# Kernel optimization log

Measured on AMD Instinct MI355X. Metric: run time of the kernel, lower is better.

Reference implementation:

```python
import jax, jax.numpy as jnp
import numpy as np

N_NODES = 50000
N_EDGES = 800000
D = 128          # embedding_dim
G = 3            # group_size
K = 4            # window_size
ALPHA = -0.5
WEIGHTS = (1.0, 1.0, 7.81, 45.28)
EPS = 1e-12      # torch F.normalize clamp_min


def _striped_projection(key):
    """Striped sparse random projection, densified (matches torch coalesce+to_dense)."""
    num_groups = D // G  # 42; columns 126..127 remain zero, as in the original
    k_off, k_sign = jax.random.split(key)
    row_idx = jnp.repeat(jnp.arange(N_NODES), num_groups)
    base = jnp.tile(jnp.arange(0, num_groups * G, G), N_NODES)
    off = jax.random.randint(k_off, (N_NODES * num_groups,), 0, G)
    col_idx = base + off
    scale = float(np.sqrt(G))  # 1/sqrt(density), density = 1/g
    vals = (jax.random.randint(k_sign, (N_NODES * num_groups,), 0, 2).astype(jnp.float32) * 2.0 - 1.0) * scale
    return jnp.zeros((N_NODES, D), jnp.float32).at[row_idx, col_idx].add(vals)


def setup_inputs() -> dict:
    key = jax.random.key(0)
    k1, k2, k3 = jax.random.split(key, 3)
    edge_row = jax.random.randint(k1, (N_EDGES,), 0, N_NODES)
    edge_col = jax.random.randint(k2, (N_EDGES,), 0, N_NODES)
    edge_val = jnp.ones((N_EDGES,), jnp.float32)
    R = _striped_projection(k3)
    return {"edge_row": edge_row, "edge_col": edge_col, "edge_val": edge_val, "R": R}


def reference(edge_row, edge_col, edge_val, R):
    N = R.shape[0]
    # degrees = row sums of sparse adjacency; zeros -> 1
    deg = jax.ops.segment_sum(edge_val, edge_row, num_segments=N)
    deg = jnp.where(deg == 0, 1.0, deg)
    # initial degree scaling: N_curr = R * deg**alpha
    x = R * (deg ** ALPHA)[:, None]
    inv_deg = (1.0 / deg)[:, None]
    acc = jnp.zeros_like(R)
    for i in range(K):
        # SpMM: out[r] = sum_{e: row[e]==r} val[e] * x[col[e]]
        x = jax.ops.segment_sum(edge_val[:, None] * x[edge_col], edge_row, num_segments=N)
        x = x * inv_deg  # transition-matrix ('trans') scaling
        nrm = jnp.maximum(jnp.sqrt(jnp.sum(x * x, axis=1, keepdims=True)), EPS)
        acc = acc + (x / nrm) * WEIGHTS[i]
    mean = acc.mean(axis=0)
    std = jnp.std(acc, axis=0, ddof=1)  # torch .std() is unbiased
    std = jnp.where(std == 0, 1.0, std)
    return (acc - mean) / std
```

## Files before the change

### kernel.cpp

```cpp
#include <hip/hip_runtime.h>
#include <math.h>

#define NN 50000
#define NE 800000
#define DD 128
#define NBKT 196
#define BCAP 5120
#define CHUNK 2048
#define NCHUNK ((NE + CHUNK - 1) / CHUNK)
#define CS1_NBLK 1024
#define CS_ROWS 49

static __device__ __forceinline__ float blo(unsigned int p) { return __uint_as_float(p << 16); }
static __device__ __forceinline__ float bhi(unsigned int p) { return __uint_as_float(p & 0xffff0000u); }
static __device__ __forceinline__ unsigned int pack2bf(float a, float b) {
    unsigned int ua = __float_as_uint(a);
    unsigned int ub = __float_as_uint(b);
    ua = ua + 0x7FFFu + ((ua >> 16) & 1u);
    ub = ub + 0x7FFFu + ((ub >> 16) & 1u);
    return (ua >> 16) | (ub & 0xffff0000u);
}

static __global__ __launch_bounds__(256) void bin_kernel(
    const int* __restrict__ erow, const int* __restrict__ ecol, const float* __restrict__ eval_,
    int* __restrict__ bucket_cursor, uint2* __restrict__ binned) {
    __shared__ uint2 sorted[CHUNK];
    __shared__ unsigned short sbin[CHUNK];
    __shared__ int hist[NBKT];
    __shared__ int bstart[NBKT];
    __shared__ int bcur[NBKT];
    __shared__ int gbase[NBKT];
    __shared__ int tmp[256];

    int t = threadIdx.x;
    int cbase = blockIdx.x * CHUNK;
    int cn = NE - cbase; if (cn > CHUNK) cn = CHUNK;

    for (int i = t; i < NBKT; i += 256) hist[i] = 0;
    __syncthreads();

    unsigned int rc[8]; unsigned int vv[8]; int bb[8];
    int nloc = 0;
    for (int i = t; i < cn; i += 256) {
        int g = cbase + i;
        int r = erow[g];
        int c = ecol[g];
        float v = eval_[g];
        rc[nloc] = (unsigned)r | ((unsigned)c << 16);
        vv[nloc] = __float_as_uint(v);
        int b = r >> 8;
        bb[nloc] = b;
        atomicAdd(&hist[b], 1);
        ++nloc;
    }
    __syncthreads();

    int hv = (t < NBKT) ? hist[t] : 0;
    tmp[t] = hv;
    __syncthreads();
    for (int off = 1; off < 256; off <<= 1) {
        int u = (t >= off) ? tmp[t - off] : 0;
        __syncthreads();
        tmp[t] += u;
        __syncthreads();
    }
    if (t < NBKT) {
        int ex = tmp[t] - hv;
        bstart[t] = ex;
        bcur[t] = ex;
        gbase[t] = atomicAdd(&bucket_cursor[t], hv);
    }
    __syncthreads();

    for (int k = 0; k < nloc; ++k) {
        int pos = atomicAdd(&bcur[bb[k]], 1);
        sorted[pos] = make_uint2(rc[k], vv[k]);
        sbin[pos] = (unsigned short)bb[k];
    }
    __syncthreads();

    for (int i = t; i < cn; i += 256) {
        int b = sbin[i];
        binned[(size_t)b * BCAP + gbase[b] + (i - bstart[b])] = sorted[i];
    }
}

static __global__ void bucket_scan_kernel(const int* __restrict__ bucket_cursor,
                                          int* __restrict__ bucket_base) {
    __shared__ int tmp[256];
    int t = threadIdx.x;
    int v = (t < NBKT) ? bucket_cursor[t] : 0;
    tmp[t] = v;
    __syncthreads();
    for (int off = 1; off < 256; off <<= 1) {
        int u = (t >= off) ? tmp[t - off] : 0;
        __syncthreads();
        tmp[t] += u;
        __syncthreads();
    }
    if (t < NBKT) bucket_base[t] = tmp[t] - v;
}

static __global__ __launch_bounds__(256) void sort_kernel(
    const uint2* __restrict__ binned, const int* __restrict__ bucket_cursor,
    const int* __restrict__ bucket_base, uint2* __restrict__ csr, int* __restrict__ row_start,
    float* __restrict__ deg) {
    __shared__ uint2 buf[BCAP];
    __shared__ int hist[256];
    __shared__ int rcur[256];
    __shared__ float fdeg[256];
    int b = blockIdx.x;
    int t = threadIdx.x;
    int cnt = bucket_cursor[b];
    int gb = bucket_base[b];
    int lo = b << 8;

    hist[t] = 0;
    fdeg[t] = 0.0f;
    __syncthreads();
    for (int i = t; i < cnt; i += 256) {
        uint2 e = binned[(size_t)b * BCAP + i];
        buf[i] = e;
        int rr = (int)(e.x & 0xFFFFu) - lo;
        atomicAdd(&hist[rr], 1);
        atomicAdd(&fdeg[rr], __uint_as_float(e.y));
    }
    __syncthreads();
    int hv = hist[t];
    rcur[t] = hv;
    __syncthreads();
    for (int off = 1; off < 256; off <<= 1) {
        int u = (t >= off) ? rcur[t - off] : 0;
        __syncthreads();
        rcur[t] += u;
        __syncthreads();
    }
    int excl = rcur[t] - hv;
    int r = lo + t;
    if (r < NN) {
        row_start[r] = gb + excl;
        float d = fdeg[t];
        deg[r] = (d == 0.0f) ? 1.0f : d;
    }
    if (b == NBKT - 1 && t == 255) row_start[NN] = gb + cnt;
    rcur[t] = excl;
    __syncthreads();
    for (int i = t; i < cnt; i += 256) {
        uint2 e = buf[i];
        int rr = (int)(e.x & 0xFFFFu) - lo;
        int pos = atomicAdd(&rcur[rr], 1);
        csr[(size_t)gb + pos] = make_uint2(e.x >> 16, e.y);
    }
}

static __global__ void init_x_kernel(const float* __restrict__ R, const float* __restrict__ deg,
                                     uint4* __restrict__ xq, int nquads) {
    int i = blockIdx.x * blockDim.x + threadIdx.x;
    if (i < nquads) {
        float d = deg[i >> 4];
        float sc = rsqrtf(d);
        const float4* R4 = (const float4*)R;
        float4 f0 = R4[i * 2];
        float4 f1 = R4[i * 2 + 1];
        xq[i] = make_uint4(pack2bf(f0.x * sc, f0.y * sc), pack2bf(f0.z * sc, f0.w * sc),
                           pack2bf(f1.x * sc, f1.y * sc), pack2bf(f1.z * sc, f1.w * sc));
    }
}

static __global__ __launch_bounds__(256) void spmm_fused_kernel(
    const int* __restrict__ row_start, const uint2* __restrict__ csr,
    const uint4* __restrict__ x4, const float* __restrict__ deg,
    uint4* __restrict__ x_next4, float* __restrict__ s_out, float weight) {
    int wave = threadIdx.x >> 6;
    int lane = threadIdx.x & 63;
    int quarter = lane >> 4;
    int sub = lane & 15;
    int row = blockIdx.x * 16 + wave * 4 + quarter;
    int s = row_start[row];
    int e = row_start[row + 1];

    float a0 = 0.f, a1 = 0.f, a2 = 0.f, a3 = 0.f, a4 = 0.f, a5 = 0.f, a6 = 0.f, a7 = 0.f;
    for (int base = s; base < e; base += 16) {
        int j = base + sub;
        int cl = 0;
        float vl = 0.0f;
        if (j < e) { uint2 t2 = csr[j]; cl = (int)t2.x; vl = __uint_as_float(t2.y); }
        int cnt = e - base; if (cnt > 16) cnt = 16;
        for (int k = 0; k < cnt; k += 4) {
            int l0 = quarter * 16 + k;
            int c0 = __shfl(cl, l0);
            int c1 = __shfl(cl, l0 + 1);
            int c2 = __shfl(cl, l0 + 2);
            int c3 = __shfl(cl, l0 + 3);
            float v0 = __shfl(vl, l0);
            float v1 = __shfl(vl, l0 + 1);
            float v2 = __shfl(vl, l0 + 2);
            float v3 = __shfl(vl, l0 + 3);
            uint4 p0 = x4[(size_t)c0 * 16 + sub];
            uint4 p1 = x4[(size_t)c1 * 16 + sub];
            uint4 p2 = x4[(size_t)c2 * 16 + sub];
            uint4 p3 = x4[(size_t)c3 * 16 + sub];
            a0 += v0 * blo(p0.x); a1 += v0 * bhi(p0.x); a2 += v0 * blo(p0.y); a3 += v0 * bhi(p0.y);
            a4 += v0 * blo(p0.z); a5 += v0 * bhi(p0.z); a6 += v0 * blo(p0.w); a7 += v0 * bhi(p0.w);
            a0 += v1 * blo(p1.x); a1 += v1 * bhi(p1.x); a2 += v1 * blo(p1.y); a3 += v1 * bhi(p1.y);
            a4 += v1 * blo(p1.z); a5 += v1 * bhi(p1.z); a6 += v1 * blo(p1.w); a7 += v1 * bhi(p1.w);
            a0 += v2 * blo(p2.x); a1 += v2 * bhi(p2.x); a2 += v2 * blo(p2.y); a3 += v2 * bhi(p2.y);
            a4 += v2 * blo(p2.z); a5 += v2 * bhi(p2.z); a6 += v2 * blo(p2.w); a7 += v2 * bhi(p2.w);
            a0 += v3 * blo(p3.x); a1 += v3 * bhi(p3.x); a2 += v3 * blo(p3.y); a3 += v3 * bhi(p3.y);
            a4 += v3 * blo(p3.z); a5 += v3 * bhi(p3.z); a6 += v3 * blo(p3.w); a7 += v3 * bhi(p3.w);
        }
    }

    float id = 1.0f / deg[row];
    a0 *= id; a1 *= id; a2 *= id; a3 *= id; a4 *= id; a5 *= id; a6 *= id; a7 *= id;

    float ss = a0 * a0 + a1 * a1 + a2 * a2 + a3 * a3 + a4 * a4 + a5 * a5 + a6 * a6 + a7 * a7;
#pragma unroll
    for (int m = 1; m <= 8; m <<= 1) ss += __shfl_xor(ss, m);
    float nrm = fmaxf(sqrtf(ss), 1e-12f);

    x_next4[(size_t)row * 16 + sub] = make_uint4(pack2bf(a0, a1), pack2bf(a2, a3),
                                                 pack2bf(a4, a5), pack2bf(a6, a7));
    if (sub == 0) s_out[row] = weight / nrm;
}

static __global__ __launch_bounds__(256) void stats_kernel(
    const uint4* __restrict__ x1, const uint4* __restrict__ x2,
    const uint4* __restrict__ x3, const uint4* __restrict__ x4,
    const float* __restrict__ s1, const float* __restrict__ s2,
    const float* __restrict__ s3, const float* __restrict__ s4,
    double* __restrict__ psum, double* __restrict__ psumsq) {
    __shared__ double shs[256 * 8];
    __shared__ double shq[256 * 8];
    int t = threadIdx.x;
    int sub = t & 15;
    int ro = t >> 4;
    int rbeg = blockIdx.x * CS_ROWS;
    int rend = rbeg + CS_ROWS; if (rend > NN) rend = NN;

    double ls[8], lq[8];
#pragma unroll
    for (int j = 0; j < 8; ++j) { ls[j] = 0.0; lq[j] = 0.0; }

    for (int r = rbeg + ro; r < rend; r += 16) {
        float w1 = s1[r], w2 = s2[r], w3 = s3[r], w4 = s4[r];
        size_t xi = (size_t)r * 16 + sub;
        uint4 q1 = x1[xi], q2 = x2[xi], q3 = x3[xi], q4 = x4[xi];
        float v[8];
        v[0] = w1 * blo(q1.x) + w2 * blo(q2.x) + w3 * blo(q3.x) + w4 * blo(q4.x);
        v[1] = w1 * bhi(q1.x) + w2 * bhi(q2.x) + w3 * bhi(q3.x) + w4 * bhi(q4.x);
        v[2] = w1 * blo(q1.y) + w2 * blo(q2.y) + w3 * blo(q3.y) + w4 * blo(q4.y);
        v[3] = w1 * bhi(q1.y) + w2 * bhi(q2.y) + w3 * bhi(q3.y) + w4 * bhi(q4.y);
        v[4] = w1 * blo(q1.z) + w2 * blo(q2.z) + w3 * blo(q3.z) + w4 * blo(q4.z);
        v[5] = w1 * bhi(q1.z) + w2 * bhi(q2.z) + w3 * bhi(q3.z) + w4 * bhi(q4.z);
        v[6] = w1 * blo(q1.w) + w2 * blo(q2.w) + w3 * blo(q3.w) + w4 * blo(q4.w);
        v[7] = w1 * bhi(q1.w) + w2 * bhi(q2.w) + w3 * bhi(q3.w) + w4 * bhi(q4.w);
#pragma unroll
        for (int j = 0; j < 8; ++j) { ls[j] += (double)v[j]; lq[j] += (double)v[j] * (double)v[j]; }
    }
#pragma unroll
    for (int j = 0; j < 8; ++j) { shs[t * 8 + j] = ls[j]; shq[t * 8 + j] = lq[j]; }
    __syncthreads();
    if (t < DD) {
        int cs = t >> 3, cj = t & 7;
        double s = 0.0, q = 0.0;
        for (int g = 0; g < 16; ++g) {
            int src = (g * 16 + cs) * 8 + cj;
            s += shs[src];
            q += shq[src];
        }
        psum[(size_t)blockIdx.x * DD + t] = s;
        psumsq[(size_t)blockIdx.x * DD + t] = q;
    }
}

static __global__ __launch_bounds__(256) void colstats_fold_kernel(
    const double* __restrict__ psum, const double* __restrict__ psumsq,
    float* __restrict__ mean, float* __restrict__ invstd) {
    __shared__ double ss[256], qq[256];
    int c = blockIdx.x;
    int t = threadIdx.x;
    double s = 0.0, q = 0.0;
    for (int b = t; b < CS1_NBLK; b += 256) {
        s += psum[(size_t)b * DD + c];
        q += psumsq[(size_t)b * DD + c];
    }
    ss[t] = s; qq[t] = q;
    __syncthreads();
    for (int off = 128; off > 0; off >>= 1) {
        if (t < off) { ss[t] += ss[t + off]; qq[t] += qq[t + off]; }
        __syncthreads();
    }
    if (t == 0) {
        double m = ss[0] / (double)NN;
        double var = (qq[0] - (double)NN * m * m) / (double)(NN - 1);
        if (var < 0.0) var = 0.0;
        double sd = sqrt(var);
        if (sd == 0.0) sd = 1.0;
        mean[c] = (float)m;
        invstd[c] = (float)(1.0 / sd);
    }
}

static __global__ __launch_bounds__(256) void final_kernel(
    const uint4* __restrict__ x1, const uint4* __restrict__ x2,
    const uint4* __restrict__ x3, const uint4* __restrict__ x4,
    const float* __restrict__ s1, const float* __restrict__ s2,
    const float* __restrict__ s3, const float* __restrict__ s4,
    const float* __restrict__ mean, const float* __restrict__ invstd,
    float* __restrict__ out) {
    int i = blockIdx.x * blockDim.x + threadIdx.x;
    int r = i >> 4;
    int sub = i & 15;
    float w1 = s1[r], w2 = s2[r], w3 = s3[r], w4 = s4[r];
    uint4 q1 = x1[i], q2 = x2[i], q3 = x3[i], q4 = x4[i];
    float v[8];
    v[0] = w1 * blo(q1.x) + w2 * blo(q2.x) + w3 * blo(q3.x) + w4 * blo(q4.x);
    v[1] = w1 * bhi(q1.x) + w2 * bhi(q2.x) + w3 * bhi(q3.x) + w4 * bhi(q4.x);
    v[2] = w1 * blo(q1.y) + w2 * blo(q2.y) + w3 * blo(q3.y) + w4 * blo(q4.y);
    v[3] = w1 * bhi(q1.y) + w2 * bhi(q2.y) + w3 * bhi(q3.y) + w4 * bhi(q4.y);
    v[4] = w1 * blo(q1.z) + w2 * blo(q2.z) + w3 * blo(q3.z) + w4 * blo(q4.z);
    v[5] = w1 * bhi(q1.z) + w2 * bhi(q2.z) + w3 * bhi(q3.z) + w4 * bhi(q4.z);
    v[6] = w1 * blo(q1.w) + w2 * blo(q2.w) + w3 * blo(q3.w) + w4 * blo(q4.w);
    v[7] = w1 * bhi(q1.w) + w2 * bhi(q2.w) + w3 * bhi(q3.w) + w4 * bhi(q4.w);
    const float4* m4 = (const float4*)mean;
    const float4* is4 = (const float4*)invstd;
    float4 m0 = m4[sub * 2], m1 = m4[sub * 2 + 1];
    float4 i0 = is4[sub * 2], i1 = is4[sub * 2 + 1];
    float4* out4 = (float4*)out;
    out4[(size_t)i * 2]     = make_float4((v[0] - m0.x) * i0.x, (v[1] - m0.y) * i0.y,
                                          (v[2] - m0.z) * i0.z, (v[3] - m0.w) * i0.w);
    out4[(size_t)i * 2 + 1] = make_float4((v[4] - m1.x) * i1.x, (v[5] - m1.y) * i1.y,
                                          (v[6] - m1.z) * i1.z, (v[7] - m1.w) * i1.w);
}

extern "C" void kernel_launch(void* const* d_in, const int* in_sizes, int n_in,
                              void* d_out, int out_size, void* d_ws, size_t ws_size,
                              hipStream_t stream) {
    const int* erow = (const int*)d_in[0];
    const int* ecol = (const int*)d_in[1];
    const float* eval_ = (const float*)d_in[2];
    const float* R = (const float*)d_in[3];
    float* out = (float*)d_out;

    char* ws = (char*)d_ws;
    size_t off = 0;
    auto alloc = [&](size_t bytes) -> char* {
        char* p = ws + off;
        off += (bytes + 255) & ~(size_t)255;
        return p;
    };
    float* deg          = (float*)alloc(NN * sizeof(float));
    int* bucket_cursor  = (int*)alloc(NBKT * sizeof(int));
    int* bucket_base    = (int*)alloc(NBKT * sizeof(int));
    int* row_start      = (int*)alloc((NN + 1) * sizeof(int));
    uint2* binned       = (uint2*)alloc((size_t)NBKT * BCAP * sizeof(uint2));
    uint2* csr          = (uint2*)alloc((size_t)NE * sizeof(uint2));
    uint4* x0           = (uint4*)alloc((size_t)NN * 16 * sizeof(uint4));
    uint4* x1           = (uint4*)alloc((size_t)NN * 16 * sizeof(uint4));
    uint4* x2           = (uint4*)alloc((size_t)NN * 16 * sizeof(uint4));
    uint4* x3           = (uint4*)alloc((size_t)NN * 16 * sizeof(uint4));
    uint4* x4           = (uint4*)alloc((size_t)NN * 16 * sizeof(uint4));
    float* s1           = (float*)alloc(NN * sizeof(float));
    float* s2           = (float*)alloc(NN * sizeof(float));
    float* s3           = (float*)alloc(NN * sizeof(float));
    float* s4           = (float*)alloc(NN * sizeof(float));
    double* psum        = (double*)alloc((size_t)CS1_NBLK * DD * sizeof(double));
    double* psumsq      = (double*)alloc((size_t)CS1_NBLK * DD * sizeof(double));
    float* meanbuf      = (float*)alloc(DD * sizeof(float));
    float* invstdb      = (float*)alloc(DD * sizeof(float));

    hipMemsetAsync(bucket_cursor, 0, NBKT * sizeof(int), stream);

    const int total = NN * DD;
    const int nquads = total / 8;

    bin_kernel<<<NCHUNK, 256, 0, stream>>>(erow, ecol, eval_, bucket_cursor, binned);
    bucket_scan_kernel<<<1, 256, 0, stream>>>(bucket_cursor, bucket_base);
    sort_kernel<<<NBKT, 256, 0, stream>>>(binned, bucket_cursor, bucket_base, csr, row_start, deg);

    init_x_kernel<<<(nquads + 255) / 256, 256, 0, stream>>>(R, deg, x0, nquads);

    spmm_fused_kernel<<<NN / 16, 256, 0, stream>>>(row_start, csr, x0, deg, x1, s1, 1.0f);
    spmm_fused_kernel<<<NN / 16, 256, 0, stream>>>(row_start, csr, x1, deg, x2, s2, 1.0f);
    spmm_fused_kernel<<<NN / 16, 256, 0, stream>>>(row_start, csr, x2, deg, x3, s3, 7.81f);
    spmm_fused_kernel<<<NN / 16, 256, 0, stream>>>(row_start, csr, x3, deg, x4, s4, 45.28f);

    stats_kernel<<<CS1_NBLK, 256, 0, stream>>>(x1, x2, x3, x4, s1, s2, s3, s4, psum, psumsq);
    colstats_fold_kernel<<<DD, 256, 0, stream>>>(psum, psumsq, meanbuf, invstdb);
    final_kernel<<<NN * 16 / 256, 256, 0, stream>>>(x1, x2, x3, x4, s1, s2, s3, s4,
                                                    meanbuf, invstdb, out);
}
```

Measured before the change: 253.4 us.

## Fuse bucket scan and x0 init into sort; fuse stats and accumulation into last SpMM

Each sort block now computes the bucket prefix scan itself and writes its own rows of the degree-scaled bf16 x0, so the separate scan and init kernels go away. The last SpMM iteration builds the weighted sum of all four hops in place of storing x4. It writes the unnormalized result to out and emits per-block float column partial sums. A light normalize pass then rescales out in place, removing the extra re-reads of x1..x4 by the separate stats and final kernels. The per-block partials are now float instead of double, which may cost a little accuracy in the variance.

```diff
diff --git a/kernel.cpp b/kernel.cpp
--- a/kernel.cpp
+++ b/kernel.cpp
@@ -8,8 +8,7 @@
 #define BCAP 5120
 #define CHUNK 2048
 #define NCHUNK ((NE + CHUNK - 1) / CHUNK)
-#define CS1_NBLK 1024
-#define CS_ROWS 49
+#define SPMM_NBLK (NN / 16)
 
 static __device__ __forceinline__ float blo(unsigned int p) { return __uint_as_float(p << 16); }
 static __device__ __forceinline__ float bhi(unsigned int p) { return __uint_as_float(p & 0xffff0000u); }
@@ -85,39 +84,33 @@
     }
 }
 
-static __global__ void bucket_scan_kernel(const int* __restrict__ bucket_cursor,
-                                          int* __restrict__ bucket_base) {
-    __shared__ int tmp[256];
-    int t = threadIdx.x;
-    int v = (t < NBKT) ? bucket_cursor[t] : 0;
-    tmp[t] = v;
-    __syncthreads();
-    for (int off = 1; off < 256; off <<= 1) {
-        int u = (t >= off) ? tmp[t - off] : 0;
-        __syncthreads();
-        tmp[t] += u;
-        __syncthreads();
-    }
-    if (t < NBKT) bucket_base[t] = tmp[t] - v;
-}
-
 static __global__ __launch_bounds__(256) void sort_kernel(
     const uint2* __restrict__ binned, const int* __restrict__ bucket_cursor,
-    const int* __restrict__ bucket_base, uint2* __restrict__ csr, int* __restrict__ row_start,
-    float* __restrict__ deg) {
+    uint2* __restrict__ csr, int* __restrict__ row_start, float* __restrict__ deg,
+    const float* __restrict__ R, uint4* __restrict__ x0) {
     __shared__ uint2 buf[BCAP];
     __shared__ int hist[256];
     __shared__ int rcur[256];
     __shared__ float fdeg[256];
+    __shared__ int pscan[256];
     int b = blockIdx.x;
     int t = threadIdx.x;
-    int cnt = bucket_cursor[b];
-    int gb = bucket_base[b];
     int lo = b << 8;
 
+    int pv = (t < NBKT) ? bucket_cursor[t] : 0;
+    pscan[t] = pv;
     hist[t] = 0;
     fdeg[t] = 0.0f;
     __syncthreads();
+    for (int off = 1; off < 256; off <<= 1) {
+        int u = (t >= off) ? pscan[t - off] : 0;
+        __syncthreads();
+        pscan[t] += u;
+        __syncthreads();
+    }
+    int gb = (b == 0) ? 0 : pscan[b - 1];
+    int cnt = pscan[b] - gb;
+
     for (int i = t; i < cnt; i += 256) {
         uint2 e = binned[(size_t)b * BCAP + i];
         buf[i] = e;
@@ -151,18 +144,19 @@
         int pos = atomicAdd(&rcur[rr], 1);
         csr[(size_t)gb + pos] = make_uint2(e.x >> 16, e.y);
     }
-}
-
-static __global__ void init_x_kernel(const float* __restrict__ R, const float* __restrict__ deg,
-                                     uint4* __restrict__ xq, int nquads) {
-    int i = blockIdx.x * blockDim.x + threadIdx.x;
-    if (i < nquads) {
-        float d = deg[i >> 4];
+
+    int nrows = NN - lo; if (nrows > 256) nrows = 256;
+    const float4* __restrict__ R4 = (const float4*)R;
+    for (int idx = t; idx < nrows * 16; idx += 256) {
+        int rr = idx >> 4;
+        int sub = idx & 15;
+        float d = fdeg[rr];
+        d = (d == 0.0f) ? 1.0f : d;
         float sc = rsqrtf(d);
-        const float4* R4 = (const float4*)R;
-        float4 f0 = R4[i * 2];
-        float4 f1 = R4[i * 2 + 1];
-        xq[i] = make_uint4(pack2bf(f0.x * sc, f0.y * sc), pack2bf(f0.z * sc, f0.w * sc),
+        size_t g = (size_t)(lo + rr) * 16 + sub;
+        float4 f0 = R4[g * 2];
+        float4 f1 = R4[g * 2 + 1];
+        x0[g] = make_uint4(pack2bf(f0.x * sc, f0.y * sc), pack2bf(f0.z * sc, f0.w * sc),
                            pack2bf(f1.x * sc, f1.y * sc), pack2bf(f1.z * sc, f1.w * sc));
     }
 }
@@ -224,66 +218,110 @@
     if (sub == 0) s_out[row] = weight / nrm;
 }
 
-static __global__ __launch_bounds__(256) void stats_kernel(
-    const uint4* __restrict__ x1, const uint4* __restrict__ x2,
-    const uint4* __restrict__ x3, const uint4* __restrict__ x4,
-    const float* __restrict__ s1, const float* __restrict__ s2,
-    const float* __restrict__ s3, const float* __restrict__ s4,
-    double* __restrict__ psum, double* __restrict__ psumsq) {
-    __shared__ double shs[256 * 8];
-    __shared__ double shq[256 * 8];
+static __global__ __launch_bounds__(256) void spmm_last_kernel(
+    const int* __restrict__ row_start, const uint2* __restrict__ csr,
+    const uint4* __restrict__ xin, const float* __restrict__ deg,
+    const uint4* __restrict__ x1, const uint4* __restrict__ x2, const uint4* __restrict__ x3,
+    const float* __restrict__ s1, const float* __restrict__ s2, const float* __restrict__ s3,
+    float* __restrict__ out, float* __restrict__ psum, float* __restrict__ psumsq, float weight) {
+    __shared__ float shs[256 * 8];
+    __shared__ float shq[256 * 8];
+    int wave = threadIdx.x >> 6;
+    int lane = threadIdx.x & 63;
+    int quarter = lane >> 4;
+    int sub = lane & 15;
+    int row = blockIdx.x * 16 + wave * 4 + quarter;
+    int s = row_start[row];
+    int e = row_start[row + 1];
+
+    float a0 = 0.f, a1 = 0.f, a2 = 0.f, a3 = 0.f, a4 = 0.f, a5 = 0.f, a6 = 0.f, a7 = 0.f;
+    for (int base = s; base < e; base += 16) {
+        int j = base + sub;
+        int cl = 0;
+        float vl = 0.0f;
+        if (j < e) { uint2 t2 = csr[j]; cl = (int)t2.x; vl = __uint_as_float(t2.y); }
+        int cnt = e - base; if (cnt > 16) cnt = 16;
+        for (int k = 0; k < cnt; k += 4) {
+            int l0 = quarter * 16 + k;
+            int c0 = __shfl(cl, l0);
+            int c1 = __shfl(cl, l0 + 1);
+            int c2 = __shfl(cl, l0 + 2);
+            int c3 = __shfl(cl, l0 + 3);
+            float v0 = __shfl(vl, l0);
+            float v1 = __shfl(vl, l0 + 1);
+            float v2 = __shfl(vl, l0 + 2);
+            float v3 = __shfl(vl, l0 + 3);
+            uint4 p0 = xin[(size_t)c0 * 16 + sub];
+            uint4 p1 = xin[(size_t)c1 * 16 + sub];
+            uint4 p2 = xin[(size_t)c2 * 16 + sub];
+            uint4 p3 = xin[(size_t)c3 * 16 + sub];
+            a0 += v0 * blo(p0.x); a1 += v0 * bhi(p0.x); a2 += v0 * blo(p0.y); a3 += v0 * bhi(p0.y);
+            a4 += v0 * blo(p0.z); a5 += v0 * bhi(p0.z); a6 += v0 * blo(p0.w); a7 += v0 * bhi(p0.w);
+            a0 += v1 * blo(p1.x); a1 += v1 * bhi(p1.x); a2 += v1 * blo(p1.y); a3 += v1 * bhi(p1.y);
+            a4 += v1 * blo(p1.z); a5 += v1 * bhi(p1.z); a6 += v1 * blo(p1.w); a7 += v1 * bhi(p1.w);
+            a0 += v2 * blo(p2.x); a1 += v2 * bhi(p2.x); a2 += v2 * blo(p2.y); a3 += v2 * bhi(p2.y);
+            a4 += v2 * blo(p2.z); a5 += v2 * bhi(p2.z); a6 += v2 * blo(p2.w); a7 += v2 * bhi(p2.w);
+            a0 += v3 * blo(p3.x); a1 += v3 * bhi(p3.x); a2 += v3 * blo(p3.y); a3 += v3 * bhi(p3.y);
+            a4 += v3 * blo(p3.z); a5 += v3 * bhi(p3.z); a6 += v3 * blo(p3.w); a7 += v3 * bhi(p3.w);
+        }
+    }
+
+    float id = 1.0f / deg[row];
+    a0 *= id; a1 *= id; a2 *= id; a3 *= id; a4 *= id; a5 *= id; a6 *= id; a7 *= id;
+
+    float ss = a0 * a0 + a1 * a1 + a2 * a2 + a3 * a3 + a4 * a4 + a5 * a5 + a6 * a6 + a7 * a7;
+#pragma unroll
+    for (int m = 1; m <= 8; m <<= 1) ss += __shfl_xor(ss, m);
+    float nrm = fmaxf(sqrtf(ss), 1e-12f);
+    float w4 = weight / nrm;
+
+    size_t xi = (size_t)row * 16 + sub;
+    float w1 = s1[row], w2 = s2[row], w3 = s3[row];
+    uint4 q1 = x1[xi], q2 = x2[xi], q3 = x3[xi];
+    float v[8];
+    v[0] = w1 * blo(q1.x) + w2 * blo(q2.x) + w3 * blo(q3.x) + w4 * a0;
+    v[1] = w1 * bhi(q1.x) + w2 * bhi(q2.x) + w3 * bhi(q3.x) + w4 * a1;
+    v[2] = w1 * blo(q1.y) + w2 * blo(q2.y) + w3 * blo(q3.y) + w4 * a2;
+    v[3] = w1 * bhi(q1.y) + w2 * bhi(q2.y) + w3 * bhi(q3.y) + w4 * a3;
+    v[4] = w1 * blo(q1.z) + w2 * blo(q2.z) + w3 * blo(q3.z) + w4 * a4;
+    v[5] = w1 * bhi(q1.z) + w2 * bhi(q2.z) + w3 * bhi(q3.z) + w4 * a5;
+    v[6] = w1 * blo(q1.w) + w2 * blo(q2.w) + w3 * blo(q3.w) + w4 * a6;
+    v[7] = w1 * bhi(q1.w) + w2 * bhi(q2.w) + w3 * bhi(q3.w) + w4 * a7;
+
+    float4* out4 = (float4*)out;
+    out4[(size_t)row * 32 + sub * 2]     = make_float4(v[0], v[1], v[2], v[3]);
+    out4[(size_t)row * 32 + sub * 2 + 1] = make_float4(v[4], v[5], v[6], v[7]);
+
     int t = threadIdx.x;
-    int sub = t & 15;
-    int ro = t >> 4;
-    int rbeg = blockIdx.x * CS_ROWS;
-    int rend = rbeg + CS_ROWS; if (rend > NN) rend = NN;
-
-    double ls[8], lq[8];
 #pragma unroll
-    for (int j = 0; j < 8; ++j) { ls[j] = 0.0; lq[j] = 0.0; }
-
-    for (int r = rbeg + ro; r < rend; r += 16) {
-        float w1 = s1[r], w2 = s2[r], w3 = s3[r], w4 = s4[r];
-        size_t xi = (size_t)r * 16 + sub;
-        uint4 q1 = x1[xi], q2 = x2[xi], q3 = x3[xi], q4 = x4[xi];
-        float v[8];
-        v[0] = w1 * blo(q1.x) + w2 * blo(q2.x) + w3 * blo(q3.x) + w4 * blo(q4.x);
-        v[1] = w1 * bhi(q1.x) + w2 * bhi(q2.x) + w3 * bhi(q3.x) + w4 * bhi(q4.x);
-        v[2] = w1 * blo(q1.y) + w2 * blo(q2.y) + w3 * blo(q3.y) + w4 * blo(q4.y);
-        v[3] = w1 * bhi(q1.y) + w2 * bhi(q2.y) + w3 * bhi(q3.y) + w4 * bhi(q4.y);
-        v[4] = w1 * blo(q1.z) + w2 * blo(q2.z) + w3 * blo(q3.z) + w4 * blo(q4.z);
-        v[5] = w1 * bhi(q1.z) + w2 * bhi(q2.z) + w3 * bhi(q3.z) + w4 * bhi(q4.z);
-        v[6] = w1 * blo(q1.w) + w2 * blo(q2.w) + w3 * blo(q3.w) + w4 * blo(q4.w);
-        v[7] = w1 * bhi(q1.w) + w2 * bhi(q2.w) + w3 * bhi(q3.w) + w4 * bhi(q4.w);
-#pragma unroll
-        for (int j = 0; j < 8; ++j) { ls[j] += (double)v[j]; lq[j] += (double)v[j] * (double)v[j]; }
-    }
-#pragma unroll
-    for (int j = 0; j < 8; ++j) { shs[t * 8 + j] = ls[j]; shq[t * 8 + j] = lq[j]; }
+    for (int j = 0; j < 8; ++j) {
+        shs[t * 8 + j] = v[j];
+        shq[t * 8 + j] = v[j] * v[j];
+    }
     __syncthreads();
     if (t < DD) {
         int cs = t >> 3, cj = t & 7;
-        double s = 0.0, q = 0.0;
+        float sacc = 0.0f, qacc = 0.0f;
         for (int g = 0; g < 16; ++g) {
             int src = (g * 16 + cs) * 8 + cj;
-            s += shs[src];
-            q += shq[src];
+            sacc += shs[src];
+            qacc += shq[src];
         }
-        psum[(size_t)blockIdx.x * DD + t] = s;
-        psumsq[(size_t)blockIdx.x * DD + t] = q;
-    }
-}
-
-static __global__ __launch_bounds__(256) void colstats_fold_kernel(
-    const double* __restrict__ psum, const double* __restrict__ psumsq,
+        psum[(size_t)blockIdx.x * DD + t] = sacc;
+        psumsq[(size_t)blockIdx.x * DD + t] = qacc;
+    }
+}
+
+static __global__ __launch_bounds__(256) void fold_kernel(
+    const float* __restrict__ psum, const float* __restrict__ psumsq,
     float* __restrict__ mean, float* __restrict__ invstd) {
     __shared__ double ss[256], qq[256];
     int c = blockIdx.x;
     int t = threadIdx.x;
     double s = 0.0, q = 0.0;
-    for (int b = t; b < CS1_NBLK; b += 256) {
-        s += psum[(size_t)b * DD + c];
-        q += psumsq[(size_t)b * DD + c];
+    for (int b = t; b < SPMM_NBLK; b += 256) {
+        s += (double)psum[(size_t)b * DD + c];
+        q += (double)psumsq[(size_t)b * DD + c];
     }
     ss[t] = s; qq[t] = q;
     __syncthreads();
@@ -302,36 +340,19 @@
     }
 }
 
-static __global__ __launch_bounds__(256) void final_kernel(
-    const uint4* __restrict__ x1, const uint4* __restrict__ x2,
-    const uint4* __restrict__ x3, const uint4* __restrict__ x4,
-    const float* __restrict__ s1, const float* __restrict__ s2,
-    const float* __restrict__ s3, const float* __restrict__ s4,
-    const float* __restrict__ mean, const float* __restrict__ invstd,
-    float* __restrict__ out) {
+static __global__ __launch_bounds__(256) void normalize_kernel(
+    float* __restrict__ out, const float* __restrict__ mean, const float* __restrict__ invstd) {
     int i = blockIdx.x * blockDim.x + threadIdx.x;
-    int r = i >> 4;
-    int sub = i & 15;
-    float w1 = s1[r], w2 = s2[r], w3 = s3[r], w4 = s4[r];
-    uint4 q1 = x1[i], q2 = x2[i], q3 = x3[i], q4 = x4[i];
-    float v[8];
-    v[0] = w1 * blo(q1.x) + w2 * blo(q2.x) + w3 * blo(q3.x) + w4 * blo(q4.x);
-    v[1] = w1 * bhi(q1.x) + w2 * bhi(q2.x) + w3 * bhi(q3.x) + w4 * bhi(q4.x);
-    v[2] = w1 * blo(q1.y) + w2 * blo(q2.y) + w3 * blo(q3.y) + w4 * blo(q4.y);
-    v[3] = w1 * bhi(q1.y) + w2 * bhi(q2.y) + w3 * bhi(q3.y) + w4 * bhi(q4.y);
-    v[4] = w1 * blo(q1.z) + w2 * blo(q2.z) + w3 * blo(q3.z) + w4 * blo(q4.z);
-    v[5] = w1 * bhi(q1.z) + w2 * bhi(q2.z) + w3 * bhi(q3.z) + w4 * bhi(q4.z);
-    v[6] = w1 * blo(q1.w) + w2 * blo(q2.w) + w3 * blo(q3.w) + w4 * blo(q4.w);
-    v[7] = w1 * bhi(q1.w) + w2 * bhi(q2.w) + w3 * bhi(q3.w) + w4 * bhi(q4.w);
-    const float4* m4 = (const float4*)mean;
-    const float4* is4 = (const float4*)invstd;
-    float4 m0 = m4[sub * 2], m1 = m4[sub * 2 + 1];
-    float4 i0 = is4[sub * 2], i1 = is4[sub * 2 + 1];
+    int c4 = i & 31;
+    float4 m = ((const float4*)mean)[c4];
+    float4 is = ((const float4*)invstd)[c4];
     float4* out4 = (float4*)out;
-    out4[(size_t)i * 2]     = make_float4((v[0] - m0.x) * i0.x, (v[1] - m0.y) * i0.y,
-                                          (v[2] - m0.z) * i0.z, (v[3] - m0.w) * i0.w);
-    out4[(size_t)i * 2 + 1] = make_float4((v[4] - m1.x) * i1.x, (v[5] - m1.y) * i1.y,
-                                          (v[6] - m1.z) * i1.z, (v[7] - m1.w) * i1.w);
+    float4 v = out4[i];
+    v.x = (v.x - m.x) * is.x;
+    v.y = (v.y - m.y) * is.y;
+    v.z = (v.z - m.z) * is.z;
+    v.w = (v.w - m.w) * is.w;
+    out4[i] = v;
 }
 
 extern "C" void kernel_launch(void* const* d_in, const int* in_sizes, int n_in,
@@ -352,7 +373,6 @@
     };
     float* deg          = (float*)alloc(NN * sizeof(float));
     int* bucket_cursor  = (int*)alloc(NBKT * sizeof(int));
-    int* bucket_base    = (int*)alloc(NBKT * sizeof(int));
     int* row_start      = (int*)alloc((NN + 1) * sizeof(int));
     uint2* binned       = (uint2*)alloc((size_t)NBKT * BCAP * sizeof(uint2));
     uint2* csr          = (uint2*)alloc((size_t)NE * sizeof(uint2));
@@ -360,34 +380,25 @@
     uint4* x1           = (uint4*)alloc((size_t)NN * 16 * sizeof(uint4));
     uint4* x2           = (uint4*)alloc((size_t)NN * 16 * sizeof(uint4));
     uint4* x3           = (uint4*)alloc((size_t)NN * 16 * sizeof(uint4));
-    uint4* x4           = (uint4*)alloc((size_t)NN * 16 * sizeof(uint4));
     float* s1           = (float*)alloc(NN * sizeof(float));
     float* s2           = (float*)alloc(NN * sizeof(float));
     float* s3           = (float*)alloc(NN * sizeof(float));
-    float* s4           = (float*)alloc(NN * sizeof(float));
-    double* psum        = (double*)alloc((size_t)CS1_NBLK * DD * sizeof(double));
-    double* psumsq      = (double*)alloc((size_t)CS1_NBLK * DD * sizeof(double));
+    float* psum         = (float*)alloc((size_t)SPMM_NBLK * DD * sizeof(float));
+    float* psumsq       = (float*)alloc((size_t)SPMM_NBLK * DD * sizeof(float));
     float* meanbuf      = (float*)alloc(DD * sizeof(float));
     float* invstdb      = (float*)alloc(DD * sizeof(float));
 
     hipMemsetAsync(bucket_cursor, 0, NBKT * sizeof(int), stream);
 
-    const int total = NN * DD;
-    const int nquads = total / 8;
-
     bin_kernel<<<NCHUNK, 256, 0, stream>>>(erow, ecol, eval_, bucket_cursor, binned);
-    bucket_scan_kernel<<<1, 256, 0, stream>>>(bucket_cursor, bucket_base);
-    sort_kernel<<<NBKT, 256, 0, stream>>>(binned, bucket_cursor, bucket_base, csr, row_start, deg);
-
-    init_x_kernel<<<(nquads + 255) / 256, 256, 0, stream>>>(R, deg, x0, nquads);
-
-    spmm_fused_kernel<<<NN / 16, 256, 0, stream>>>(row_start, csr, x0, deg, x1, s1, 1.0f);
-    spmm_fused_kernel<<<NN / 16, 256, 0, stream>>>(row_start, csr, x1, deg, x2, s2, 1.0f);
-    spmm_fused_kernel<<<NN / 16, 256, 0, stream>>>(row_start, csr, x2, deg, x3, s3, 7.81f);
-    spmm_fused_kernel<<<NN / 16, 256, 0, stream>>>(row_start, csr, x3, deg, x4, s4, 45.28f);
-
-    stats_kernel<<<CS1_NBLK, 256, 0, stream>>>(x1, x2, x3, x4, s1, s2, s3, s4, psum, psumsq);
-    colstats_fold_kernel<<<DD, 256, 0, stream>>>(psum, psumsq, meanbuf, invstdb);
-    final_kernel<<<NN * 16 / 256, 256, 0, stream>>>(x1, x2, x3, x4, s1, s2, s3, s4,
-                                                    meanbuf, invstdb, out);
-}
+    sort_kernel<<<NBKT, 256, 0, stream>>>(binned, bucket_cursor, csr, row_start, deg, R, x0);
+
+    spmm_fused_kernel<<<SPMM_NBLK, 256, 0, stream>>>(row_start, csr, x0, deg, x1, s1, 1.0f);
+    spmm_fused_kernel<<<SPMM_NBLK, 256, 0, stream>>>(row_start, csr, x1, deg, x2, s2, 1.0f);
+    spmm_fused_kernel<<<SPMM_NBLK, 256, 0, stream>>>(row_start, csr, x2, deg, x3, s3, 7.81f);
+    spmm_last_kernel<<<SPMM_NBLK, 256, 0, stream>>>(row_start, csr, x3, deg, x1, x2, x3,
+                                                    s1, s2, s3, out, psum, psumsq, 45.28f);
+
+    fold_kernel<<<DD, 256, 0, stream>>>(psum, psumsq, meanbuf, invstdb);
+    normalize_kernel<<<NN * 32 / 256, 256, 0, stream>>>(out, meanbuf, invstdb);
+}
```

After: 252.0 us. About the same (-0.6%).

## Split SpMM into column slices, fold bucket scan and init into sort kernel

Applied to the files above, without the earlier changes.

The SpMM is restructured so each row is handled by 4 lanes, and the grid is split into 4 column slices of 32 features each. Within a launch, each slice gathers only a quarter of every source row, which is meant to shrink the working set and improve L2 reuse. Per-slice partial squared norms are written out and combined by a new small kernel that computes the per-row scale factors. Separately, the bucket prefix scan and the x0 initialisation are folded into the sort kernel, and the output stores become nontemporal. The cost is that each slice re-reads the CSR indices, and the extra partial-norm buffer adds memory traffic.

```diff
diff --git a/kernel.cpp b/kernel.cpp
--- a/kernel.cpp
+++ b/kernel.cpp
@@ -8,8 +8,12 @@
 #define BCAP 5120
 #define CHUNK 2048
 #define NCHUNK ((NE + CHUNK - 1) / CHUNK)
+#define NSLICE 4
+#define RB ((NN + 63) / 64)
 #define CS1_NBLK 1024
 #define CS_ROWS 49
+
+typedef unsigned int uiv4 __attribute__((ext_vector_type(4)));
 
 static __device__ __forceinline__ float blo(unsigned int p) { return __uint_as_float(p << 16); }
 static __device__ __forceinline__ float bhi(unsigned int p) { return __uint_as_float(p & 0xffff0000u); }
@@ -85,39 +89,33 @@
     }
 }
 
-static __global__ void bucket_scan_kernel(const int* __restrict__ bucket_cursor,
-                                          int* __restrict__ bucket_base) {
-    __shared__ int tmp[256];
-    int t = threadIdx.x;
-    int v = (t < NBKT) ? bucket_cursor[t] : 0;
-    tmp[t] = v;
-    __syncthreads();
-    for (int off = 1; off < 256; off <<= 1) {
-        int u = (t >= off) ? tmp[t - off] : 0;
-        __syncthreads();
-        tmp[t] += u;
-        __syncthreads();
-    }
-    if (t < NBKT) bucket_base[t] = tmp[t] - v;
-}
-
 static __global__ __launch_bounds__(256) void sort_kernel(
     const uint2* __restrict__ binned, const int* __restrict__ bucket_cursor,
-    const int* __restrict__ bucket_base, uint2* __restrict__ csr, int* __restrict__ row_start,
-    float* __restrict__ deg) {
+    uint2* __restrict__ csr, int* __restrict__ row_start, float* __restrict__ deg,
+    const float* __restrict__ R, uint4* __restrict__ x0) {
     __shared__ uint2 buf[BCAP];
     __shared__ int hist[256];
     __shared__ int rcur[256];
     __shared__ float fdeg[256];
+    __shared__ int pscan[256];
     int b = blockIdx.x;
     int t = threadIdx.x;
-    int cnt = bucket_cursor[b];
-    int gb = bucket_base[b];
     int lo = b << 8;
 
+    int pv = (t < NBKT) ? bucket_cursor[t] : 0;
+    pscan[t] = pv;
     hist[t] = 0;
     fdeg[t] = 0.0f;
     __syncthreads();
+    for (int off = 1; off < 256; off <<= 1) {
+        int u = (t >= off) ? pscan[t - off] : 0;
+        __syncthreads();
+        pscan[t] += u;
+        __syncthreads();
+    }
+    int gb = (b == 0) ? 0 : pscan[b - 1];
+    int cnt = pscan[b] - gb;
+
     for (int i = t; i < cnt; i += 256) {
         uint2 e = binned[(size_t)b * BCAP + i];
         buf[i] = e;
@@ -151,63 +149,76 @@
         int pos = atomicAdd(&rcur[rr], 1);
         csr[(size_t)gb + pos] = make_uint2(e.x >> 16, e.y);
     }
-}
-
-static __global__ void init_x_kernel(const float* __restrict__ R, const float* __restrict__ deg,
-                                     uint4* __restrict__ xq, int nquads) {
-    int i = blockIdx.x * blockDim.x + threadIdx.x;
-    if (i < nquads) {
-        float d = deg[i >> 4];
+
+    int nrows = NN - lo; if (nrows > 256) nrows = 256;
+    const float4* __restrict__ R4 = (const float4*)R;
+    for (int idx = t; idx < nrows * 16; idx += 256) {
+        int rr = idx >> 4;
+        int sub = idx & 15;
+        float d = fdeg[rr];
+        d = (d == 0.0f) ? 1.0f : d;
         float sc = rsqrtf(d);
-        const float4* R4 = (const float4*)R;
-        float4 f0 = R4[i * 2];
-        float4 f1 = R4[i * 2 + 1];
-        xq[i] = make_uint4(pack2bf(f0.x * sc, f0.y * sc), pack2bf(f0.z * sc, f0.w * sc),
+        size_t g = (size_t)(lo + rr) * 16 + sub;
+        float4 f0 = R4[g * 2];
+        float4 f1 = R4[g * 2 + 1];
+        x0[g] = make_uint4(pack2bf(f0.x * sc, f0.y * sc), pack2bf(f0.z * sc, f0.w * sc),
                            pack2bf(f1.x * sc, f1.y * sc), pack2bf(f1.z * sc, f1.w * sc));
     }
 }
 
-static __global__ __launch_bounds__(256) void spmm_fused_kernel(
+static __global__ __launch_bounds__(256) void spmm_slice_kernel(
     const int* __restrict__ row_start, const uint2* __restrict__ csr,
-    const uint4* __restrict__ x4, const float* __restrict__ deg,
-    uint4* __restrict__ x_next4, float* __restrict__ s_out, float weight) {
-    int wave = threadIdx.x >> 6;
-    int lane = threadIdx.x & 63;
-    int quarter = lane >> 4;
-    int sub = lane & 15;
-    int row = blockIdx.x * 16 + wave * 4 + quarter;
+    const uint4* __restrict__ xin, const float* __restrict__ deg,
+    uint4* __restrict__ xout, float* __restrict__ ssp) {
+    int slice = blockIdx.x / RB;
+    int blk = blockIdx.x - slice * RB;
+    int t = threadIdx.x;
+    int l4 = t & 3;
+    int row = blk * 64 + (t >> 2);
+    if (row >= NN) return;
+    int wb = (t & 63) & ~3;
     int s = row_start[row];
     int e = row_start[row + 1];
+    int sl4 = slice * 4 + l4;
 
     float a0 = 0.f, a1 = 0.f, a2 = 0.f, a3 = 0.f, a4 = 0.f, a5 = 0.f, a6 = 0.f, a7 = 0.f;
-    for (int base = s; base < e; base += 16) {
-        int j = base + sub;
-        int cl = 0;
-        float vl = 0.0f;
+    int base = s;
+    for (; base + 4 <= e; base += 4) {
+        uint2 t2 = csr[base + l4];
+        int cl = (int)t2.x;
+        float vl = __uint_as_float(t2.y);
+        int c0 = __shfl(cl, wb);
+        int c1 = __shfl(cl, wb + 1);
+        int c2 = __shfl(cl, wb + 2);
+        int c3 = __shfl(cl, wb + 3);
+        float v0 = __shfl(vl, wb);
+        float v1 = __shfl(vl, wb + 1);
+        float v2 = __shfl(vl, wb + 2);
+        float v3 = __shfl(vl, wb + 3);
+        uint4 p0 = xin[(size_t)c0 * 16 + sl4];
+        uint4 p1 = xin[(size_t)c1 * 16 + sl4];
+        uint4 p2 = xin[(size_t)c2 * 16 + sl4];
+        uint4 p3 = xin[(size_t)c3 * 16 + sl4];
+        a0 += v0 * blo(p0.x); a1 += v0 * bhi(p0.x); a2 += v0 * blo(p0.y); a3 += v0 * bhi(p0.y);
+        a4 += v0 * blo(p0.z); a5 += v0 * bhi(p0.z); a6 += v0 * blo(p0.w); a7 += v0 * bhi(p0.w);
+        a0 += v1 * blo(p1.x); a1 += v1 * bhi(p1.x); a2 += v1 * blo(p1.y); a3 += v1 * bhi(p1.y);
+        a4 += v1 * blo(p1.z); a5 += v1 * bhi(p1.z); a6 += v1 * blo(p1.w); a7 += v1 * bhi(p1.w);
+        a0 += v2 * blo(p2.x); a1 += v2 * bhi(p2.x); a2 += v2 * blo(p2.y); a3 += v2 * bhi(p2.y);
+        a4 += v2 * blo(p2.z); a5 += v2 * bhi(p2.z); a6 += v2 * blo(p2.w); a7 += v2 * bhi(p2.w);
+        a0 += v3 * blo(p3.x); a1 += v3 * bhi(p3.x); a2 += v3 * blo(p3.y); a3 += v3 * bhi(p3.y);
+        a4 += v3 * blo(p3.z); a5 += v3 * bhi(p3.z); a6 += v3 * blo(p3.w); a7 += v3 * bhi(p3.w);
+    }
+    if (base < e) {
+        int j = base + l4;
+        int cl = 0; float vl = 0.0f;
         if (j < e) { uint2 t2 = csr[j]; cl = (int)t2.x; vl = __uint_as_float(t2.y); }
-        int cnt = e - base; if (cnt > 16) cnt = 16;
-        for (int k = 0; k < cnt; k += 4) {
-            int l0 = quarter * 16 + k;
-            int c0 = __shfl(cl, l0);
-            int c1 = __shfl(cl, l0 + 1);
-            int c2 = __shfl(cl, l0 + 2);
-            int c3 = __shfl(cl, l0 + 3);
-            float v0 = __shfl(vl, l0);
-            float v1 = __shfl(vl, l0 + 1);
-            float v2 = __shfl(vl, l0 + 2);
-            float v3 = __shfl(vl, l0 + 3);
-            uint4 p0 = x4[(size_t)c0 * 16 + sub];
-            uint4 p1 = x4[(size_t)c1 * 16 + sub];
-            uint4 p2 = x4[(size_t)c2 * 16 + sub];
-            uint4 p3 = x4[(size_t)c3 * 16 + sub];
-            a0 += v0 * blo(p0.x); a1 += v0 * bhi(p0.x); a2 += v0 * blo(p0.y); a3 += v0 * bhi(p0.y);
-            a4 += v0 * blo(p0.z); a5 += v0 * bhi(p0.z); a6 += v0 * blo(p0.w); a7 += v0 * bhi(p0.w);
-            a0 += v1 * blo(p1.x); a1 += v1 * bhi(p1.x); a2 += v1 * blo(p1.y); a3 += v1 * bhi(p1.y);
-            a4 += v1 * blo(p1.z); a5 += v1 * bhi(p1.z); a6 += v1 * blo(p1.w); a7 += v1 * bhi(p1.w);
-            a0 += v2 * blo(p2.x); a1 += v2 * bhi(p2.x); a2 += v2 * blo(p2.y); a3 += v2 * bhi(p2.y);
-            a4 += v2 * blo(p2.z); a5 += v2 * bhi(p2.z); a6 += v2 * blo(p2.w); a7 += v2 * bhi(p2.w);
-            a0 += v3 * blo(p3.x); a1 += v3 * bhi(p3.x); a2 += v3 * blo(p3.y); a3 += v3 * bhi(p3.y);
-            a4 += v3 * blo(p3.z); a5 += v3 * bhi(p3.z); a6 += v3 * blo(p3.w); a7 += v3 * bhi(p3.w);
+        int cnt = e - base;
+        for (int k = 0; k < cnt; ++k) {
+            int c = __shfl(cl, wb + k);
+            float v = __shfl(vl, wb + k);
+            uint4 p = xin[(size_t)c * 16 + sl4];
+            a0 += v * blo(p.x); a1 += v * bhi(p.x); a2 += v * blo(p.y); a3 += v * bhi(p.y);
+            a4 += v * blo(p.z); a5 += v * bhi(p.z); a6 += v * blo(p.w); a7 += v * bhi(p.w);
         }
     }
 
@@ -215,13 +226,29 @@
     a0 *= id; a1 *= id; a2 *= id; a3 *= id; a4 *= id; a5 *= id; a6 *= id; a7 *= id;
 
     float ss = a0 * a0 + a1 * a1 + a2 * a2 + a3 * a3 + a4 * a4 + a5 * a5 + a6 * a6 + a7 * a7;
+    ss += __shfl_xor(ss, 1);
+    ss += __shfl_xor(ss, 2);
+
+    uiv4 o = { pack2bf(a0, a1), pack2bf(a2, a3), pack2bf(a4, a5), pack2bf(a6, a7) };
+    __builtin_nontemporal_store(o, (uiv4*)&xout[(size_t)row * 16 + sl4]);
+    if (l4 == 0) ssp[(size_t)slice * NN + row] = ss;
+}
+
+static __global__ __launch_bounds__(256) void s_kernel(
+    const float* __restrict__ ssp,
+    float* __restrict__ s1, float* __restrict__ s2,
+    float* __restrict__ s3, float* __restrict__ s4) {
+    int r = blockIdx.x * blockDim.x + threadIdx.x;
+    if (r >= NN) return;
+    const float w[4] = {1.0f, 1.0f, 7.81f, 45.28f};
+    float* sout[4] = {s1, s2, s3, s4};
 #pragma unroll
-    for (int m = 1; m <= 8; m <<= 1) ss += __shfl_xor(ss, m);
-    float nrm = fmaxf(sqrtf(ss), 1e-12f);
-
-    x_next4[(size_t)row * 16 + sub] = make_uint4(pack2bf(a0, a1), pack2bf(a2, a3),
-                                                 pack2bf(a4, a5), pack2bf(a6, a7));
-    if (sub == 0) s_out[row] = weight / nrm;
+    for (int h = 0; h < 4; ++h) {
+        const float* p = ssp + (size_t)h * NSLICE * NN;
+        float ss = p[r] + p[NN + r] + p[2 * NN + r] + p[3 * NN + r];
+        float nrm = fmaxf(sqrtf(ss), 1e-12f);
+        sout[h][r] = w[h] / nrm;
+    }
 }
 
 static __global__ __launch_bounds__(256) void stats_kernel(
@@ -274,7 +301,7 @@
     }
 }
 
-static __global__ __launch_bounds__(256) void colstats_fold_kernel(
+static __global__ __launch_bounds__(256) void fold_kernel(
     const double* __restrict__ psum, const double* __restrict__ psumsq,
     float* __restrict__ mean, float* __restrict__ invstd) {
     __shared__ double ss[256], qq[256];
@@ -352,7 +379,6 @@
     };
     float* deg          = (float*)alloc(NN * sizeof(float));
     int* bucket_cursor  = (int*)alloc(NBKT * sizeof(int));
-    int* bucket_base    = (int*)alloc(NBKT * sizeof(int));
     int* row_start      = (int*)alloc((NN + 1) * sizeof(int));
     uint2* binned       = (uint2*)alloc((size_t)NBKT * BCAP * sizeof(uint2));
     uint2* csr          = (uint2*)alloc((size_t)NE * sizeof(uint2));
@@ -361,6 +387,7 @@
     uint4* x2           = (uint4*)alloc((size_t)NN * 16 * sizeof(uint4));
     uint4* x3           = (uint4*)alloc((size_t)NN * 16 * sizeof(uint4));
     uint4* x4           = (uint4*)alloc((size_t)NN * 16 * sizeof(uint4));
+    float* ssp          = (float*)alloc((size_t)4 * NSLICE * NN * sizeof(float));
     float* s1           = (float*)alloc(NN * sizeof(float));
     float* s2           = (float*)alloc(NN * sizeof(float));
     float* s3           = (float*)alloc(NN * sizeof(float));
@@ -372,22 +399,22 @@
 
     hipMemsetAsync(bucket_cursor, 0, NBKT * sizeof(int), stream);
 
-    const int total = NN * DD;
-    const int nquads = total / 8;
-
     bin_kernel<<<NCHUNK, 256, 0, stream>>>(erow, ecol, eval_, bucket_cursor, binned);
-    bucket_scan_kernel<<<1, 256, 0, stream>>>(bucket_cursor, bucket_base);
-    sort_kernel<<<NBKT, 256, 0, stream>>>(binned, bucket_cursor, bucket_base, csr, row_start, deg);
-
-    init_x_kernel<<<(nquads + 255) / 256, 256, 0, stream>>>(R, deg, x0, nquads);
-
-    spmm_fused_kernel<<<NN / 16, 256, 0, stream>>>(row_start, csr, x0, deg, x1, s1, 1.0f);
-    spmm_fused_kernel<<<NN / 16, 256, 0, stream>>>(row_start, csr, x1, deg, x2, s2, 1.0f);
-    spmm_fused_kernel<<<NN / 16, 256, 0, stream>>>(row_start, csr, x2, deg, x3, s3, 7.81f);
-    spmm_fused_kernel<<<NN / 16, 256, 0, stream>>>(row_start, csr, x3, deg, x4, s4, 45.28f);
-
+    sort_kernel<<<NBKT, 256, 0, stream>>>(binned, bucket_cursor, csr, row_start, deg, R, x0);
+
+    const int hop_grid = NSLICE * RB;
+    spmm_slice_kernel<<<hop_grid, 256, 0, stream>>>(row_start, csr, x0, deg, x1,
+                                                    ssp + 0 * NSLICE * NN);
+    spmm_slice_kernel<<<hop_grid, 256, 0, stream>>>(row_start, csr, x1, deg, x2,
+                                                    ssp + 1 * NSLICE * NN);
+    spmm_slice_kernel<<<hop_grid, 256, 0, stream>>>(row_start, csr, x2, deg, x3,
+                                                    ssp + 2 * NSLICE * NN);
+    spmm_slice_kernel<<<hop_grid, 256, 0, stream>>>(row_start, csr, x3, deg, x4,
+                                                    ssp + 3 * NSLICE * NN);
+
+    s_kernel<<<(NN + 255) / 256, 256, 0, stream>>>(ssp, s1, s2, s3, s4);
     stats_kernel<<<CS1_NBLK, 256, 0, stream>>>(x1, x2, x3, x4, s1, s2, s3, s4, psum, psumsq);
-    colstats_fold_kernel<<<DD, 256, 0, stream>>>(psum, psumsq, meanbuf, invstdb);
+    fold_kernel<<<DD, 256, 0, stream>>>(psum, psumsq, meanbuf, invstdb);
     final_kernel<<<NN * 16 / 256, 256, 0, stream>>>(x1, x2, x3, x4, s1, s2, s3, s4,
                                                     meanbuf, invstdb, out);
 }
```

Result: slower. 341.8 us (+34.9%).
